# Performance work log

Measured on AMD Instinct MI355X. Metric: run time of the kernel, lower is better.

## Reference

```python
import jax, jax.numpy as jnp
import numpy as np

N_NODES = 100000
N_EDGES = 1600000
IN_DIM = 256
OUT_DIM = 32


def setup_inputs() -> dict:
    key = jax.random.key(0)
    k1, k2, k3, k4, k5 = jax.random.split(key, 5)
    x = jax.random.normal(k1, (N_NODES, IN_DIM), dtype=jnp.float32)
    src = jax.random.randint(k2, (N_EDGES,), 0, N_NODES, dtype=jnp.int32)
    dst = jax.random.randint(k3, (N_EDGES,), 0, N_NODES, dtype=jnp.int32)
    # GraphConv parameters (DGL: weight [in, out], bias [out])
    W = jax.random.normal(k4, (IN_DIM, OUT_DIM), dtype=jnp.float32) / np.sqrt(IN_DIM)
    b = jnp.zeros((OUT_DIM,), dtype=jnp.float32)
    return {"x": x, "src": src, "dst": dst, "W": W, "b": b}


def reference(x, src, dst, W, b):
    # DGL GraphConv, norm='both', allow_zero_in_degree=True:
    #   out = D_in^{-1/2} A D_out^{-1/2} X W + b  (degrees clamped to min 1)
    ones = jnp.ones(src.shape[0], dtype=x.dtype)
    deg_out = jax.ops.segment_sum(ones, src, num_segments=N_NODES)
    deg_in = jax.ops.segment_sum(ones, dst, num_segments=N_NODES)
    norm_src = jnp.clip(deg_out, 1.0, None) ** -0.5  # [N]
    norm_dst = jnp.clip(deg_in, 1.0, None) ** -0.5   # [N]
    # in_dim > out_dim: project first (smaller messages), then aggregate
    h = (x * norm_src[:, None]) @ W                  # [N, out]
    msgs = h[src]                                    # [E, out] gather
    agg = jax.ops.segment_sum(msgs, dst, num_segments=N_NODES)  # [N, out]
    return agg * norm_dst[:, None] + b
```

## Files before the change

### kernel.cpp

```cpp
#include <hip/hip_runtime.h>

#define N_NODES 100000
#define N_EDGES 1600000
#define IN_DIM 256
#define OUT_DIM 32

#define SB_SHIFT 7
#define NSB ((N_NODES + 127) >> 7)
#define SBCAP 2368
#define EBLK 2048
#define NB1 ((N_EDGES + EBLK - 1) / EBLK)
#define NGB ((N_NODES + 255) / 256)

typedef __attribute__((ext_vector_type(8))) short short8;
typedef __attribute__((ext_vector_type(16))) float f32x16;

#define WT_STRIDE 264

__device__ inline unsigned short f2bf(float f) {
    unsigned u = __float_as_uint(f);
    unsigned r = u + 0x7FFF + ((u >> 16) & 1);
    return (unsigned short)(r >> 16);
}
__device__ inline float bf2f(unsigned short us) {
    return __uint_as_float((unsigned)us << 16);
}

__global__ __launch_bounds__(512) void k_mega(const int* __restrict__ src,
                                              const int* __restrict__ dst,
                                              unsigned long long* __restrict__ qcnt,
                                              unsigned* __restrict__ gsb,
                                              unsigned char* __restrict__ gss,
                                              const float* __restrict__ x,
                                              const float* __restrict__ W,
                                              unsigned short* __restrict__ h2) {
    __shared__ __align__(16) int smemI[6 * NSB + 2 * EBLK];
    const int tid = threadIdx.x;
    const int bid = blockIdx.x;
    const int g = bid / 3;
    const int rem = bid - g * 3;

    if (rem == 0) {
        unsigned short* WT = (unsigned short*)smemI;
        #pragma unroll
        for (int i = 0; i < 16; ++i) {
            int idx = tid + i * 512;
            WT[(idx & 31) * WT_STRIDE + (idx >> 5)] = f2bf(W[idx]);
        }
        __syncthreads();

        const int wv = tid >> 6;
        const int lane = tid & 63;
        const int col = lane & 31;
        const int hi = lane >> 5;

        const int row0 = g * 256 + wv * 32;
        int grow = row0 + col;
        int growc = grow < N_NODES ? grow : N_NODES - 1;
        const float4* xrow = reinterpret_cast<const float4*>(x + (size_t)growc * IN_DIM);

        f32x16 acc = {0.f,0.f,0.f,0.f,0.f,0.f,0.f,0.f,
                      0.f,0.f,0.f,0.f,0.f,0.f,0.f,0.f};

        #pragma unroll 4
        for (int t = 0; t < 16; ++t) {
            int k4 = t * 4 + hi * 2;
            float4 p0 = xrow[k4];
            float4 p1 = xrow[k4 + 1];
            short8 a;
            a[0] = (short)f2bf(p0.x); a[1] = (short)f2bf(p0.y);
            a[2] = (short)f2bf(p0.z); a[3] = (short)f2bf(p0.w);
            a[4] = (short)f2bf(p1.x); a[5] = (short)f2bf(p1.y);
            a[6] = (short)f2bf(p1.z); a[7] = (short)f2bf(p1.w);
            short8 bfr = *reinterpret_cast<const short8*>(
                &WT[col * WT_STRIDE + t * 16 + hi * 8]);
            acc = __builtin_amdgcn_mfma_f32_32x32x16_bf16(a, bfr, acc, 0, 0, 0);
        }

        #pragma unroll
        for (int r = 0; r < 16; ++r) {
            int rowi = (r & 3) + 8 * (r >> 2) + 4 * hi;
            int go = row0 + rowi;
            if (go < N_NODES)
                h2[(size_t)go * OUT_DIM + col] = f2bf(acc[r]);
        }
    } else {
        const int pb = 2 * g + rem - 1;
        int* hist    = smemI;
        int* bbase   = smemI + NSB;
        int* cur     = smemI + 2 * NSB;
        int* hist_s  = smemI + 3 * NSB;
        int* bbase_s = smemI + 4 * NSB;
        int* cur_s   = smemI + 5 * NSB;
        int* es      = smemI + 6 * NSB;
        int* ed      = smemI + 6 * NSB + EBLK;

        const int e0 = pb * EBLK;
        const int n = min(EBLK, N_EDGES - e0);

        for (int i = tid; i < NSB; i += 512) {
            hist[i] = 0; cur[i] = 0; hist_s[i] = 0; cur_s[i] = 0;
        }
        __syncthreads();

        for (int i = tid; i < n; i += 512) {
            int s = src[e0 + i];
            int d = dst[e0 + i];
            es[i] = s; ed[i] = d;
            atomicAdd(&hist[d >> SB_SHIFT], 1);
            atomicAdd(&hist_s[s >> SB_SHIFT], 1);
        }
        __syncthreads();

        for (int i = tid; i < NSB; i += 512) {
            unsigned long long pack =
                ((unsigned long long)(unsigned)hist_s[i] << 32) | (unsigned)hist[i];
            unsigned long long old = atomicAdd(&qcnt[i], pack);
            bbase[i]   = (int)(old & 0xFFFFFFFFull);
            bbase_s[i] = (int)(old >> 32);
        }
        __syncthreads();

        for (int i = tid; i < n; i += 512) {
            int d = ed[i];
            int s = es[i];
            int r = d >> SB_SHIFT;
            int lp = atomicAdd(&cur[r], 1);
            int pos = bbase[r] + lp;
            if (pos < SBCAP)
                gsb[(size_t)r * SBCAP + pos] = ((unsigned)(d & 127) << 17) | (unsigned)s;
            int rs = s >> SB_SHIFT;
            int lp2 = atomicAdd(&cur_s[rs], 1);
            int pos2 = bbase_s[rs] + lp2;
            if (pos2 < SBCAP)
                gss[(size_t)rs * SBCAP + pos2] = (unsigned char)(s & 127);
        }
    }
}

__global__ __launch_bounds__(256) void k_deg2(const int* __restrict__ qcnt2,
                                              const unsigned char* __restrict__ gss,
                                              unsigned short* __restrict__ h2) {
    __shared__ int hist[128];
    __shared__ float nrml[128];
    const int r = blockIdx.x;
    const int tid = threadIdx.x;
    if (tid < 128) hist[tid] = 0;
    __syncthreads();
    int cnt = qcnt2[2 * r + 1];
    if (cnt > SBCAP) cnt = SBCAP;
    const unsigned char* bp = gss + (size_t)r * SBCAP;
    for (int i = tid; i < cnt; i += 256)
        atomicAdd(&hist[bp[i]], 1);
    __syncthreads();
    if (tid < 128) {
        int dg = hist[tid];
        nrml[tid] = rsqrtf((float)(dg > 1 ? dg : 1));
    }
    __syncthreads();

    const int n0 = r << SB_SHIFT;
    for (int i = tid; i < 128 * 8; i += 256) {
        int row = i >> 3;
        int node = n0 + row;
        if (node < N_NODES) {
            float w = nrml[row];
            ushort4* p = reinterpret_cast<ushort4*>(&h2[(size_t)node * OUT_DIM]) + (i & 7);
            ushort4 v = *p;
            v.x = f2bf(bf2f(v.x) * w);
            v.y = f2bf(bf2f(v.y) * w);
            v.z = f2bf(bf2f(v.z) * w);
            v.w = f2bf(bf2f(v.w) * w);
            *p = v;
        }
    }
}

__global__ __launch_bounds__(512) void k_combo2(const int* __restrict__ qcnt2,
                                                const unsigned* __restrict__ gsb,
                                                const unsigned short* __restrict__ h2,
                                                const float* __restrict__ bias,
                                                float* __restrict__ out) {
    __shared__ unsigned pstage[SBCAP];
    __shared__ int esl[SBCAP];
    __shared__ int hist[128];
    __shared__ int pref[128];
    __shared__ int cur[128];

    const int r = blockIdx.x;
    const int tid = threadIdx.x;

    if (tid < 128) { hist[tid] = 0; cur[tid] = 0; }
    int cnt = qcnt2[2 * r];
    if (cnt > SBCAP) cnt = SBCAP;
    const unsigned* bp = gsb + (size_t)r * SBCAP;
    __syncthreads();

    for (int i = tid; i < cnt; i += 512) {
        unsigned pay = bp[i];
        pstage[i] = pay;
        atomicAdd(&hist[pay >> 17], 1);
    }
    __syncthreads();

    int v = 0;
    if (tid < 128) { v = hist[tid]; pref[tid] = v; }
    __syncthreads();
    #pragma unroll
    for (int off = 1; off < 128; off <<= 1) {
        int t = (tid < 128 && tid >= off) ? pref[tid - off] : 0;
        __syncthreads();
        if (tid < 128) pref[tid] += t;
        __syncthreads();
    }
    if (tid < 128) pref[tid] -= v;
    __syncthreads();

    for (int i = tid; i < cnt; i += 512) {
        unsigned pay = pstage[i];
        int l = (int)(pay >> 17);
        int lp = atomicAdd(&cur[l], 1);
        esl[pref[l] + lp] = (int)(pay & 0x1FFFF);
    }
    __syncthreads();

    const int q = tid & 7;
    const int nl = tid >> 3;
    const float4 bb = reinterpret_cast<const float4*>(bias)[q];
    #pragma unroll
    for (int sweep = 0; sweep < 2; ++sweep) {
        int l = sweep * 64 + nl;
        int st = pref[l];
        int deg = hist[l];
        float4 acc = make_float4(0.f, 0.f, 0.f, 0.f);
        int j = 0;
        for (; j + 4 <= deg; j += 4) {
            int s0 = esl[st + j + 0];
            int s1 = esl[st + j + 1];
            int s2 = esl[st + j + 2];
            int s3 = esl[st + j + 3];
            ushort4 a0 = *reinterpret_cast<const ushort4*>(&h2[(size_t)s0 * OUT_DIM + q * 4]);
            ushort4 a1 = *reinterpret_cast<const ushort4*>(&h2[(size_t)s1 * OUT_DIM + q * 4]);
            ushort4 a2 = *reinterpret_cast<const ushort4*>(&h2[(size_t)s2 * OUT_DIM + q * 4]);
            ushort4 a3 = *reinterpret_cast<const ushort4*>(&h2[(size_t)s3 * OUT_DIM + q * 4]);
            acc.x += (bf2f(a0.x) + bf2f(a1.x)) + (bf2f(a2.x) + bf2f(a3.x));
            acc.y += (bf2f(a0.y) + bf2f(a1.y)) + (bf2f(a2.y) + bf2f(a3.y));
            acc.z += (bf2f(a0.z) + bf2f(a1.z)) + (bf2f(a2.z) + bf2f(a3.z));
            acc.w += (bf2f(a0.w) + bf2f(a1.w)) + (bf2f(a2.w) + bf2f(a3.w));
        }
        for (; j < deg; ++j) {
            int s = esl[st + j];
            ushort4 a = *reinterpret_cast<const ushort4*>(&h2[(size_t)s * OUT_DIM + q * 4]);
            acc.x += bf2f(a.x); acc.y += bf2f(a.y);
            acc.z += bf2f(a.z); acc.w += bf2f(a.w);
        }
        int node = (r << SB_SHIFT) + l;
        if (node < N_NODES) {
            float nrm = rsqrtf((float)(deg > 1 ? deg : 1));
            float4 o = make_float4(acc.x * nrm + bb.x, acc.y * nrm + bb.y,
                                   acc.z * nrm + bb.z, acc.w * nrm + bb.w);
            reinterpret_cast<float4*>(out)[(size_t)node * 8 + q] = o;
        }
    }
}

extern "C" void kernel_launch(void* const* d_in, const int* in_sizes, int n_in,
                              void* d_out, int out_size, void* d_ws, size_t ws_size,
                              hipStream_t stream) {
    const float* x   = (const float*)d_in[0];
    const int*   src = (const int*)d_in[1];
    const int*   dst = (const int*)d_in[2];
    const float* W   = (const float*)d_in[3];
    const float* b   = (const float*)d_in[4];
    float* out = (float*)d_out;

    unsigned long long* qcnt = (unsigned long long*)d_ws;
    int* qcnt2 = (int*)qcnt;
    unsigned short* h2 = (unsigned short*)((char*)d_ws + 6272);
    unsigned* gsb = (unsigned*)((char*)d_ws + 6406272);
    unsigned char* gss = (unsigned char*)((char*)d_ws + 13813376);

    hipMemsetAsync(qcnt, 0, NSB * sizeof(unsigned long long), stream);

    k_mega<<<NB1 + NGB, 512, 0, stream>>>(src, dst, qcnt, gsb, gss, x, W, h2);

    k_deg2<<<NSB, 256, 0, stream>>>(qcnt2, gss, h2);

    k_combo2<<<NSB, 512, 0, stream>>>(qcnt2, gsb, h2, b, out);
}
```

Measured before the change: 82.06 us.

## Split GEMM into 32-row blocks with split-K across waves and LDS reduction

The projection GEMM blocks now each handle 32 rows instead of 256. The 8 waves split the K dimension, and partial results are reduced through LDS atomics before the bf16 store. The x tile is staged into LDS with coalesced float4 loads, and the block interleaving changes from 1 GEMM per 2 edge blocks to 4 GEMM per 1 edge block. The aim is more GEMM blocks for better parallelism and load coalescing, at the cost of reloading W per block and the extra LDS atomic reduction and barriers.

```diff
diff --git a/kernel.cpp b/kernel.cpp
--- a/kernel.cpp
+++ b/kernel.cpp
@@ -10,7 +10,7 @@
 #define SBCAP 2368
 #define EBLK 2048
 #define NB1 ((N_EDGES + EBLK - 1) / EBLK)
-#define NGB ((N_NODES + 255) / 256)
+#define NGB (N_NODES / 32)
 
 typedef __attribute__((ext_vector_type(8))) short short8;
 typedef __attribute__((ext_vector_type(16))) float f32x16;
@@ -37,15 +37,34 @@
     __shared__ __align__(16) int smemI[6 * NSB + 2 * EBLK];
     const int tid = threadIdx.x;
     const int bid = blockIdx.x;
-    const int g = bid / 3;
-    const int rem = bid - g * 3;
-
-    if (rem == 0) {
-        unsigned short* WT = (unsigned short*)smemI;
+    const int g = bid / 5;
+    const int rem = bid - g * 5;
+
+    if (rem < 4) {
+        const int gi = g * 4 + rem;
+        if (gi >= NGB) return;
+        unsigned short* WT   = (unsigned short*)smemI;
+        unsigned short* tile = (unsigned short*)(smemI + 4224);
+        float* accf          = (float*)(smemI + 4224);
+
         #pragma unroll
         for (int i = 0; i < 16; ++i) {
             int idx = tid + i * 512;
             WT[(idx & 31) * WT_STRIDE + (idx >> 5)] = f2bf(W[idx]);
+        }
+
+        const int row0 = gi * 32;
+        const float4* x4 = reinterpret_cast<const float4*>(x) + (size_t)row0 * 64;
+        #pragma unroll
+        for (int i = 0; i < 4; ++i) {
+            int j = tid + i * 512;
+            float4 v = x4[j];
+            int row = j >> 6;
+            int c4 = j & 63;
+            ushort4 w4;
+            w4.x = f2bf(v.x); w4.y = f2bf(v.y);
+            w4.z = f2bf(v.z); w4.w = f2bf(v.w);
+            *reinterpret_cast<ushort4*>(&tile[row * WT_STRIDE + c4 * 4]) = w4;
         }
         __syncthreads();
 
@@ -53,39 +72,39 @@
         const int lane = tid & 63;
         const int col = lane & 31;
         const int hi = lane >> 5;
-
-        const int row0 = g * 256 + wv * 32;
-        int grow = row0 + col;
-        int growc = grow < N_NODES ? grow : N_NODES - 1;
-        const float4* xrow = reinterpret_cast<const float4*>(x + (size_t)growc * IN_DIM);
+        const int row = col;
 
         f32x16 acc = {0.f,0.f,0.f,0.f,0.f,0.f,0.f,0.f,
                       0.f,0.f,0.f,0.f,0.f,0.f,0.f,0.f};
 
-        #pragma unroll 4
-        for (int t = 0; t < 16; ++t) {
-            int k4 = t * 4 + hi * 2;
-            float4 p0 = xrow[k4];
-            float4 p1 = xrow[k4 + 1];
-            short8 a;
-            a[0] = (short)f2bf(p0.x); a[1] = (short)f2bf(p0.y);
-            a[2] = (short)f2bf(p0.z); a[3] = (short)f2bf(p0.w);
-            a[4] = (short)f2bf(p1.x); a[5] = (short)f2bf(p1.y);
-            a[6] = (short)f2bf(p1.z); a[7] = (short)f2bf(p1.w);
-            short8 bfr = *reinterpret_cast<const short8*>(
-                &WT[col * WT_STRIDE + t * 16 + hi * 8]);
+        #pragma unroll
+        for (int t2 = 0; t2 < 2; ++t2) {
+            int kb = wv * 32 + t2 * 16 + hi * 8;
+            short8 a = *reinterpret_cast<const short8*>(&tile[row * WT_STRIDE + kb]);
+            short8 bfr = *reinterpret_cast<const short8*>(&WT[col * WT_STRIDE + kb]);
             acc = __builtin_amdgcn_mfma_f32_32x32x16_bf16(a, bfr, acc, 0, 0, 0);
         }
+        __syncthreads();
+
+        for (int i = tid; i < 32 * 33; i += 512) accf[i] = 0.f;
+        __syncthreads();
 
         #pragma unroll
         for (int r = 0; r < 16; ++r) {
             int rowi = (r & 3) + 8 * (r >> 2) + 4 * hi;
-            int go = row0 + rowi;
-            if (go < N_NODES)
-                h2[(size_t)go * OUT_DIM + col] = f2bf(acc[r]);
+            atomicAdd(&accf[rowi * 33 + col], acc[r]);
+        }
+        __syncthreads();
+
+        #pragma unroll
+        for (int p = 0; p < 2; ++p) {
+            int idx = tid + p * 512;
+            int rowi = idx >> 5;
+            int c = idx & 31;
+            h2[(size_t)(row0 + rowi) * OUT_DIM + c] = f2bf(accf[rowi * 33 + c]);
         }
     } else {
-        const int pb = 2 * g + rem - 1;
+        const int pb = g;
         int* hist    = smemI;
         int* bbase   = smemI + NSB;
         int* cur     = smemI + 2 * NSB;
@@ -282,7 +301,7 @@
 
     hipMemsetAsync(qcnt, 0, NSB * sizeof(unsigned long long), stream);
 
-    k_mega<<<NB1 + NGB, 512, 0, stream>>>(src, dst, qcnt, gsb, gss, x, W, h2);
+    k_mega<<<5 * NB1, 512, 0, stream>>>(src, dst, qcnt, gsb, gss, x, W, h2);
 
     k_deg2<<<NSB, 256, 0, stream>>>(qcnt2, gss, h2);
 
```

After: 197.8 us. +141.0%, slower.
